# Kernel tuning notes

Hardware: AMD Instinct MI355X
Metric: run time of the kernel (lower is better)

## Reference

```python
import jax, jax.numpy as jnp
import numpy as np


def _conv1x1(x, w, b):
    # x: [B,C,H,W], w: [O,C], b: [O] -> [B,O,H,W]
    return jnp.einsum('bchw,oc->bohw', x, w) + b[None, :, None, None]


def setup_inputs() -> dict:
    key = jax.random.key(0)
    ks = jax.random.split(key, 5)
    B, C, H, W = 4, 256, 64, 64
    C2 = C // 2
    scale = 0.02  # keep attention logits in a sane range
    return {
        'x': jax.random.normal(ks[0], (B, C, H, W), dtype=jnp.float32),
        'w_theta': jax.random.normal(ks[1], (C2, C), dtype=jnp.float32) * scale,
        'b_theta': jnp.zeros((C2,), dtype=jnp.float32),
        'w_phi': jax.random.normal(ks[2], (C2, C), dtype=jnp.float32) * scale,
        'b_phi': jnp.zeros((C2,), dtype=jnp.float32),
        'w_g': jax.random.normal(ks[3], (C2, C), dtype=jnp.float32) * scale,
        'b_g': jnp.zeros((C2,), dtype=jnp.float32),
        'w_out': jax.random.normal(ks[4], (C, C2), dtype=jnp.float32) * scale,
        'b_out': jnp.zeros((C,), dtype=jnp.float32),
    }


def reference(x, w_theta, b_theta, w_phi, b_phi, w_g, b_g, w_out, b_out):
    B, C, H, W = x.shape
    C2 = C // 2
    N = H * W
    theta = _conv1x1(x, w_theta, b_theta).reshape(B, C2, N)  # [B,C2,N]
    phi = _conv1x1(x, w_phi, b_phi).reshape(B, C2, N)        # [B,C2,N]
    g = _conv1x1(x, w_g, b_g).reshape(B, C2, N)              # [B,C2,N]
    # non-local attention: scores[b,m,n] = theta[b,:,m] . phi[b,:,n]
    scores = jnp.einsum('bcm,bcn->bmn', theta, phi)          # [B,N,N]
    attn = jax.nn.softmax(scores, axis=-1)                   # [B,N,N]
    # output = g @ attn^T : out[b,c,m] = sum_n g[b,c,n] * attn[b,m,n]
    out = jnp.einsum('bcn,bmn->bcm', g, attn)                # [B,C2,N]
    out = out.reshape(B, C2, H, W)
    return x + _conv1x1(out, w_out, b_out)
```

## Files before the change

kernel.cpp:

```cpp
#include <hip/hip_runtime.h>
#include <hip/hip_bf16.h>

#define B_  4
#define C_  256
#define C2_ 128
#define N_  4096
#define LOG2E 1.4426950408889634f

typedef unsigned short u16;
typedef __attribute__((ext_vector_type(8))) short bf16x8;
typedef __attribute__((ext_vector_type(4))) float f32x4;

static __device__ __forceinline__ u16 f2bf(float f) {
    return __builtin_bit_cast(u16, __float2bfloat16(f));
}
static __device__ __forceinline__ float bf2f(u16 u) {
    return __bfloat162float(__builtin_bit_cast(__hip_bfloat16, u));
}
static __device__ __forceinline__ bf16x8 cvt8(const float* p) {
    u16 t[8];
#pragma unroll
    for (int j = 0; j < 8; ++j) t[j] = f2bf(p[j]);
    return *(const bf16x8*)t;
}

__global__ __launch_bounds__(256, 2) void projx_kernel(
    const float* __restrict__ x,
    const float* __restrict__ wt, const float* __restrict__ wp,
    const float* __restrict__ wg,
    const float* __restrict__ b_theta, const float* __restrict__ b_phi,
    const float* __restrict__ b_g,
    u16* __restrict__ Q, u16* __restrict__ K, u16* __restrict__ V) {
    __shared__ __align__(16) u16 XTs[64][264];
    __shared__ __align__(16) u16 Ws[64][264];
    u16 (*Vt)[72] = (u16(*)[72])XTs;

    int bid = blockIdx.x;
    int b   = bid / (N_ / 64);
    int n0  = (bid % (N_ / 64)) * 64;
    int tid = threadIdx.x;
    int wave = tid >> 6, lane = tid & 63, quad = (lane >> 4) & 3, l16 = lane & 15;

#pragma unroll
    for (int it = 0; it < 8; ++it) {
        int idx = it * 256 + tid;
        int q = idx & 15, p = idx >> 4;
        const float* r0 = x + ((size_t)b * C_ + 2 * p) * N_ + n0 + 4 * q;
        float4 v0 = *(const float4*)r0;
        float4 v1 = *(const float4*)(r0 + N_);
        const float* f0 = (const float*)&v0;
        const float* f1 = (const float*)&v1;
#pragma unroll
        for (int j = 0; j < 4; ++j) {
            unsigned pk = (unsigned)f2bf(f0[j]) | ((unsigned)f2bf(f1[j]) << 16);
            *(unsigned*)&XTs[4 * q + j][2 * p] = pk;
        }
    }
    __syncthreads();

    bf16x8 af[8];
#pragma unroll
    for (int ks = 0; ks < 8; ++ks)
        af[ks] = *(const bf16x8*)&XTs[wave * 16 + l16][ks * 32 + quad * 8];
    __syncthreads();

    const float* wms[3]    = { wt, wp, wg };
    const float* biases[3] = { b_theta, b_phi, b_g };

#pragma unroll
    for (int mat = 0; mat < 3; ++mat) {
        const float* wm = wms[mat];
        const float* bias = biases[mat];
#pragma unroll
        for (int h = 0; h < 2; ++h) {
#pragma unroll
            for (int it = 0; it < 8; ++it) {
                int idx = it * 256 + tid;
                int row = idx >> 5, c8 = (idx & 31) * 8;
                const float* src = wm + (size_t)(h * 64 + row) * C_ + c8;
                float w8[8];
                *(float4*)&w8[0] = *(const float4*)src;
                *(float4*)&w8[4] = *(const float4*)(src + 4);
                bf16x8 v = cvt8(w8);
                *(bf16x8*)&Ws[row][c8] = v;
            }
            __syncthreads();

            f32x4 acc[4];
#pragma unroll
            for (int i = 0; i < 4; ++i) acc[i] = (f32x4){0.f, 0.f, 0.f, 0.f};
#pragma unroll
            for (int ct = 0; ct < 4; ++ct)
#pragma unroll
                for (int ks = 0; ks < 8; ++ks) {
                    bf16x8 bf = *(const bf16x8*)&Ws[ct * 16 + l16][ks * 32 + quad * 8];
                    acc[ct] = __builtin_amdgcn_mfma_f32_16x16x32_bf16(
                        af[ks], bf, acc[ct], 0, 0, 0);
                }

            if (mat < 2) {
                u16* dst = mat == 0 ? Q : K;
                float sc = mat == 0 ? LOG2E : 1.0f;
#pragma unroll
                for (int ct = 0; ct < 4; ++ct) {
                    int c2 = h * 64 + ct * 16 + l16;
                    float bb = bias[c2];
#pragma unroll
                    for (int r = 0; r < 4; ++r) {
                        int n = n0 + wave * 16 + quad * 4 + r;
                        dst[((size_t)b * N_ + n) * C2_ + c2] =
                            f2bf((acc[ct][r] + bb) * sc);
                    }
                }
            } else {
#pragma unroll
                for (int ct = 0; ct < 4; ++ct) {
                    int c2 = h * 64 + ct * 16 + l16;
                    float bb = bias[c2];
#pragma unroll
                    for (int r = 0; r < 4; ++r)
                        Vt[c2][wave * 16 + quad * 4 + r] = f2bf(acc[ct][r] + bb);
                }
            }
            __syncthreads();
        }
    }

#pragma unroll
    for (int it = 0; it < 4; ++it) {
        int idx = it * 256 + tid;
        int row = idx >> 3, n8 = (idx & 7) * 8;
        *(uint4*)(V + ((size_t)b * C2_ + row) * N_ + n0 + n8) =
            *(const uint4*)&Vt[row][n8];
    }
}

__global__ __launch_bounds__(256, 2) void attn_kernel(
    const u16* __restrict__ Q, const u16* __restrict__ K,
    const u16* __restrict__ V, u16* __restrict__ AO,
    u16* __restrict__ Opb, float* __restrict__ lsum, int nsplit) {
    const int BM = 128, BN = 64, D = C2_;
    const int per = B_ * (N_ / BM);
    int s    = blockIdx.x / per;
    int r0   = blockIdx.x % per;
    int b    = r0 / (N_ / BM);
    int m0   = (r0 % (N_ / BM)) * BM;
    int tid  = threadIdx.x;
    int wave = tid >> 6, lane = tid & 63, quad = (lane >> 4) & 3, l16 = lane & 15;

    __shared__ __align__(16) u16 Ks[BN][D + 8];
    __shared__ __align__(16) u16 Vs[D][BN + 8];
    __shared__ __align__(16) u16 Psb[4][32][BN + 8];
    u16* Ps = &Psb[wave][0][0];

    bf16x8 qf[2][4];
#pragma unroll
    for (int ms = 0; ms < 2; ++ms) {
        const u16* qp = Q + ((size_t)b * N_ + m0 + wave * 32 + ms * 16 + l16) * D;
#pragma unroll
        for (int kk = 0; kk < 4; ++kk)
            qf[ms][kk] = *(const bf16x8*)(qp + kk * 32 + quad * 8);
    }

    float l_r[2][4] = {{0.f, 0.f, 0.f, 0.f}, {0.f, 0.f, 0.f, 0.f}};
    f32x4 o_acc[2][8];
#pragma unroll
    for (int ms = 0; ms < 2; ++ms)
#pragma unroll
        for (int i = 0; i < 8; ++i) o_acc[ms][i] = (f32x4){0.f, 0.f, 0.f, 0.f};

    const int tiles = N_ / BN;
    const int base = tiles / nsplit, rem = tiles % nsplit;
    const int t0 = s * base + (s < rem ? s : rem);
    const int cnt = base + (s < rem ? 1 : 0);
    const int nt0 = t0 * BN, nt1 = (t0 + cnt) * BN;

    for (int nt = nt0; nt < nt1; nt += BN) {
        const u16* kp = K + ((size_t)b * N_ + nt) * D;
#pragma unroll
        for (int it = 0; it < 4; ++it) {
            int idx = it * 256 + tid;
            int row = idx >> 4, col = (idx & 15) * 8;
            *(uint4*)&Ks[row][col] = *(const uint4*)(kp + row * D + col);
        }
#pragma unroll
        for (int it = 0; it < 4; ++it) {
            int idx = it * 256 + tid;
            int row = idx >> 3, col = (idx & 7) * 8;
            *(uint4*)&Vs[row][col] =
                *(const uint4*)(V + ((size_t)b * C2_ + row) * N_ + nt + col);
        }
        __syncthreads();

        f32x4 sc[2][4];
#pragma unroll
        for (int nn = 0; nn < 4; ++nn) {
            f32x4 a0 = (f32x4){0.f, 0.f, 0.f, 0.f};
            f32x4 a1 = (f32x4){0.f, 0.f, 0.f, 0.f};
#pragma unroll
            for (int kk = 0; kk < 4; ++kk) {
                bf16x8 kf = *(const bf16x8*)&Ks[nn * 16 + l16][kk * 32 + quad * 8];
                a0 = __builtin_amdgcn_mfma_f32_16x16x32_bf16(qf[0][kk], kf, a0, 0, 0, 0);
                a1 = __builtin_amdgcn_mfma_f32_16x16x32_bf16(qf[1][kk], kf, a1, 0, 0, 0);
            }
            sc[0][nn] = a0;
            sc[1][nn] = a1;
        }

#pragma unroll
        for (int ms = 0; ms < 2; ++ms)
#pragma unroll
            for (int nn = 0; nn < 4; ++nn)
#pragma unroll
                for (int r = 0; r < 4; ++r) {
                    float p = __builtin_amdgcn_exp2f(sc[ms][nn][r]);
                    l_r[ms][r] += p;
                    Ps[(ms * 16 + quad * 4 + r) * (BN + 8) + nn * 16 + l16] = f2bf(p);
                }

#pragma unroll
        for (int ks = 0; ks < 2; ++ks) {
            bf16x8 pf0 = *(const bf16x8*)&Ps[(l16) * (BN + 8) + ks * 32 + quad * 8];
            bf16x8 pf1 = *(const bf16x8*)&Ps[(16 + l16) * (BN + 8) + ks * 32 + quad * 8];
#pragma unroll
            for (int cs = 0; cs < 8; ++cs) {
                bf16x8 vf = *(const bf16x8*)&Vs[cs * 16 + l16][ks * 32 + quad * 8];
                o_acc[0][cs] = __builtin_amdgcn_mfma_f32_16x16x32_bf16(pf0, vf, o_acc[0][cs], 0, 0, 0);
                o_acc[1][cs] = __builtin_amdgcn_mfma_f32_16x16x32_bf16(pf1, vf, o_acc[1][cs], 0, 0, 0);
            }
        }
        __syncthreads();
    }

#pragma unroll
    for (int ms = 0; ms < 2; ++ms)
#pragma unroll
        for (int r = 0; r < 4; ++r) {
            l_r[ms][r] += __shfl_xor(l_r[ms][r], 1);
            l_r[ms][r] += __shfl_xor(l_r[ms][r], 2);
            l_r[ms][r] += __shfl_xor(l_r[ms][r], 4);
            l_r[ms][r] += __shfl_xor(l_r[ms][r], 8);
        }

    if (Opb) {
#pragma unroll
        for (int ms = 0; ms < 2; ++ms) {
#pragma unroll
            for (int cs = 0; cs < 8; ++cs)
#pragma unroll
                for (int r = 0; r < 4; ++r) {
                    size_t row = (size_t)s * (B_ * N_) + (size_t)b * N_ +
                                 m0 + wave * 32 + ms * 16 + quad * 4 + r;
                    Opb[row * C2_ + cs * 16 + l16] = f2bf(o_acc[ms][cs][r]);
                }
            if (l16 == 0)
#pragma unroll
                for (int r = 0; r < 4; ++r) {
                    size_t row = (size_t)s * (B_ * N_) + (size_t)b * N_ +
                                 m0 + wave * 32 + ms * 16 + quad * 4 + r;
                    lsum[row] = l_r[ms][r];
                }
        }
    } else {
#pragma unroll
        for (int ms = 0; ms < 2; ++ms)
#pragma unroll
            for (int cs = 0; cs < 8; ++cs)
#pragma unroll
                for (int r = 0; r < 4; ++r) {
                    float v = o_acc[ms][cs][r] / l_r[ms][r];
                    AO[((size_t)b * N_ + m0 + wave * 32 + ms * 16 + quad * 4 + r) * C2_ +
                       cs * 16 + l16] = f2bf(v);
                }
    }
}

__global__ __launch_bounds__(256) void outproj_kernel(
    const float* __restrict__ x, const u16* __restrict__ Opb,
    const float* __restrict__ lsum, const u16* __restrict__ AO,
    const float* __restrict__ w_out, const float* __restrict__ b_out,
    float* __restrict__ y, int nsplit) {
    __shared__ __align__(16) u16 As[64][C2_ + 8];
    __shared__ __align__(16) u16 Ws2[64][C2_ + 8];
    __shared__ float Ls[64];
    int bid = blockIdx.x;
    int per_b = (C_ / 64) * (N_ / 64);
    int b   = bid / per_b;
    int rem = bid % per_b;
    int c0  = (rem / (N_ / 64)) * 64;
    int n0  = (rem % (N_ / 64)) * 64;
    int tid = threadIdx.x;
    int wave = tid >> 6, lane = tid & 63, quad = (lane >> 4) & 3, l16 = lane & 15;

#pragma unroll
    for (int it = 0; it < 4; ++it) {
        int idx = it * 256 + tid;
        int row = idx >> 4, c8 = (idx & 15) * 8;
        const float* src = w_out + (size_t)(c0 + row) * C2_ + c8;
        float w8[8];
        *(float4*)&w8[0] = *(const float4*)src;
        *(float4*)&w8[4] = *(const float4*)(src + 4);
        bf16x8 v = cvt8(w8);
        *(bf16x8*)&Ws2[row][c8] = v;
    }

    if (nsplit > 1) {
        if (tid < 64) {
            float L = 0.f;
            for (int s = 0; s < nsplit; ++s)
                L += lsum[(size_t)s * (B_ * N_) + (size_t)b * N_ + n0 + tid];
            Ls[tid] = 1.f / L;
        }
        __syncthreads();
#pragma unroll
        for (int it = 0; it < 4; ++it) {
            int idx = it * 256 + tid;
            int n = idx >> 4, c8 = (idx & 15) * 8;
            float a[8] = {0.f, 0.f, 0.f, 0.f, 0.f, 0.f, 0.f, 0.f};
            for (int s = 0; s < nsplit; ++s) {
                const u16* op = Opb +
                    ((size_t)s * (B_ * N_) + (size_t)b * N_ + n0 + n) * C2_ + c8;
                uint4 raw = *(const uint4*)op;
                const u16* rp = (const u16*)&raw;
#pragma unroll
                for (int j = 0; j < 8; ++j) a[j] += bf2f(rp[j]);
            }
            float inv = Ls[n];
            u16 o[8];
#pragma unroll
            for (int j = 0; j < 8; ++j) o[j] = f2bf(a[j] * inv);
            *(uint4*)&As[n][c8] = *(const uint4*)o;
        }
    } else {
#pragma unroll
        for (int it = 0; it < 4; ++it) {
            int idx = it * 256 + tid;
            int n = idx >> 4, c8 = (idx & 15) * 8;
            *(uint4*)&As[n][c8] =
                *(const uint4*)(AO + ((size_t)b * N_ + n0 + n) * C2_ + c8);
        }
    }
    __syncthreads();

    bf16x8 af[4];
#pragma unroll
    for (int kk = 0; kk < 4; ++kk)
        af[kk] = *(const bf16x8*)&Ws2[wave * 16 + l16][kk * 32 + quad * 8];

    f32x4 acc[4];
#pragma unroll
    for (int i = 0; i < 4; ++i) acc[i] = (f32x4){0.f, 0.f, 0.f, 0.f};

#pragma unroll
    for (int nn = 0; nn < 4; ++nn)
#pragma unroll
        for (int kk = 0; kk < 4; ++kk) {
            bf16x8 bf = *(const bf16x8*)&As[nn * 16 + l16][kk * 32 + quad * 8];
            acc[nn] = __builtin_amdgcn_mfma_f32_16x16x32_bf16(af[kk], bf, acc[nn], 0, 0, 0);
        }

    int cw = c0 + wave * 16;
    float bo[4];
#pragma unroll
    for (int r = 0; r < 4; ++r) bo[r] = b_out[cw + quad * 4 + r];

#pragma unroll
    for (int nn = 0; nn < 4; ++nn)
#pragma unroll
        for (int r = 0; r < 4; ++r) {
            int c = cw + quad * 4 + r;
            size_t off = ((size_t)b * C_ + c) * N_ + n0 + nn * 16 + l16;
            y[off] = x[off] + bo[r] + acc[nn][r];
        }
}

extern "C" void kernel_launch(void* const* d_in, const int* in_sizes, int n_in,
                              void* d_out, int out_size, void* d_ws, size_t ws_size,
                              hipStream_t stream) {
    const float* x       = (const float*)d_in[0];
    const float* w_theta = (const float*)d_in[1];
    const float* b_theta = (const float*)d_in[2];
    const float* w_phi   = (const float*)d_in[3];
    const float* b_phi   = (const float*)d_in[4];
    const float* w_g     = (const float*)d_in[5];
    const float* b_g     = (const float*)d_in[6];
    const float* w_out   = (const float*)d_in[7];
    const float* b_out   = (const float*)d_in[8];
    float* y = (float*)d_out;

    const size_t SZ = (size_t)B_ * N_ * C2_;
    u16* Q = (u16*)d_ws;
    u16* K = Q + SZ;
    u16* V = K + SZ;
    char* dyn = (char*)(V + SZ);
    size_t fixedB = 3 * SZ * 2;

    size_t perS = SZ * 2 + (size_t)B_ * N_ * 4;

    int S;
    if      (ws_size >= fixedB + 4 * perS) S = 4;
    else if (ws_size >= fixedB + 2 * perS) S = 2;
    else                                   S = 1;

    u16*   AO  = (u16*)dyn;
    u16*   Opb = nullptr;
    float* ls  = nullptr;
    if (S > 1) {
        Opb = (u16*)dyn;
        ls  = (float*)(Opb + (size_t)S * SZ);
    }

    projx_kernel<<<B_ * (N_ / 64), 256, 0, stream>>>(
        x, w_theta, w_phi, w_g, b_theta, b_phi, b_g, Q, K, V);
    attn_kernel<<<B_ * (N_ / 128) * S, 256, 0, stream>>>(Q, K, V, AO, Opb, ls, S);
    outproj_kernel<<<B_ * (C_ / 64) * (N_ / 64), 256, 0, stream>>>(
        x, Opb, ls, AO, w_out, b_out, y, S);
}
```

Measured before the change: 154.7 us.

## Split projection over channel halves, swizzle block order, coalesce output stores

```diff
diff --git a/kernel.cpp b/kernel.cpp
--- a/kernel.cpp
+++ b/kernel.cpp
@@ -23,6 +23,8 @@
     for (int j = 0; j < 8; ++j) t[j] = f2bf(p[j]);
     return *(const bf16x8*)t;
 }
+
+#define XW 264
 
 __global__ __launch_bounds__(256, 2) void projx_kernel(
     const float* __restrict__ x,
@@ -31,29 +33,31 @@
     const float* __restrict__ b_theta, const float* __restrict__ b_phi,
     const float* __restrict__ b_g,
     u16* __restrict__ Q, u16* __restrict__ K, u16* __restrict__ V) {
-    __shared__ __align__(16) u16 XTs[64][264];
-    __shared__ __align__(16) u16 Ws[64][264];
+    __shared__ __align__(16) u16 XTs[64][XW];
+    __shared__ __align__(16) u16 Ws[64][XW];
     u16 (*Vt)[72] = (u16(*)[72])XTs;
 
-    int bid = blockIdx.x;
-    int b   = bid / (N_ / 64);
-    int n0  = (bid % (N_ / 64)) * 64;
+    int p = blockIdx.x;
+    int b = (p & 7) >> 1;
+    int j = ((p >> 3) << 1) | (p & 1);
+    int h  = j >> 6;
+    int n0 = (j & 63) * 64;
     int tid = threadIdx.x;
     int wave = tid >> 6, lane = tid & 63, quad = (lane >> 4) & 3, l16 = lane & 15;
 
 #pragma unroll
     for (int it = 0; it < 8; ++it) {
         int idx = it * 256 + tid;
-        int q = idx & 15, p = idx >> 4;
-        const float* r0 = x + ((size_t)b * C_ + 2 * p) * N_ + n0 + 4 * q;
+        int q = idx & 15, pp = idx >> 4;
+        const float* r0 = x + ((size_t)b * C_ + 2 * pp) * N_ + n0 + 4 * q;
         float4 v0 = *(const float4*)r0;
         float4 v1 = *(const float4*)(r0 + N_);
         const float* f0 = (const float*)&v0;
         const float* f1 = (const float*)&v1;
 #pragma unroll
-        for (int j = 0; j < 4; ++j) {
-            unsigned pk = (unsigned)f2bf(f0[j]) | ((unsigned)f2bf(f1[j]) << 16);
-            *(unsigned*)&XTs[4 * q + j][2 * p] = pk;
+        for (int jj = 0; jj < 4; ++jj) {
+            unsigned pk = (unsigned)f2bf(f0[jj]) | ((unsigned)f2bf(f1[jj]) << 16);
+            *(unsigned*)&XTs[4 * q + jj][2 * pp] = pk;
         }
     }
     __syncthreads();
@@ -72,65 +76,61 @@
         const float* wm = wms[mat];
         const float* bias = biases[mat];
 #pragma unroll
-        for (int h = 0; h < 2; ++h) {
-#pragma unroll
-            for (int it = 0; it < 8; ++it) {
-                int idx = it * 256 + tid;
-                int row = idx >> 5, c8 = (idx & 31) * 8;
-                const float* src = wm + (size_t)(h * 64 + row) * C_ + c8;
-                float w8[8];
-                *(float4*)&w8[0] = *(const float4*)src;
-                *(float4*)&w8[4] = *(const float4*)(src + 4);
-                bf16x8 v = cvt8(w8);
-                *(bf16x8*)&Ws[row][c8] = v;
-            }
-            __syncthreads();
-
-            f32x4 acc[4];
-#pragma unroll
-            for (int i = 0; i < 4; ++i) acc[i] = (f32x4){0.f, 0.f, 0.f, 0.f};
-#pragma unroll
-            for (int ct = 0; ct < 4; ++ct)
-#pragma unroll
-                for (int ks = 0; ks < 8; ++ks) {
-                    bf16x8 bf = *(const bf16x8*)&Ws[ct * 16 + l16][ks * 32 + quad * 8];
-                    acc[ct] = __builtin_amdgcn_mfma_f32_16x16x32_bf16(
-                        af[ks], bf, acc[ct], 0, 0, 0);
+        for (int it = 0; it < 8; ++it) {
+            int idx = it * 256 + tid;
+            int row = idx >> 5, c8 = (idx & 31) * 8;
+            const float* src = wm + (size_t)(h * 64 + row) * C_ + c8;
+            float w8[8];
+            *(float4*)&w8[0] = *(const float4*)src;
+            *(float4*)&w8[4] = *(const float4*)(src + 4);
+            *(bf16x8*)&Ws[row][c8] = cvt8(w8);
+        }
+        __syncthreads();
+
+        f32x4 acc[4];
+#pragma unroll
+        for (int i = 0; i < 4; ++i) acc[i] = (f32x4){0.f, 0.f, 0.f, 0.f};
+#pragma unroll
+        for (int ct = 0; ct < 4; ++ct)
+#pragma unroll
+            for (int ks = 0; ks < 8; ++ks) {
+                bf16x8 bf = *(const bf16x8*)&Ws[ct * 16 + l16][ks * 32 + quad * 8];
+                acc[ct] = __builtin_amdgcn_mfma_f32_16x16x32_bf16(
+                    af[ks], bf, acc[ct], 0, 0, 0);
+            }
+
+        if (mat < 2) {
+            u16* dst = mat == 0 ? Q : K;
+            float scl = mat == 0 ? LOG2E : 1.0f;
+#pragma unroll
+            for (int ct = 0; ct < 4; ++ct) {
+                int c2 = h * 64 + ct * 16 + l16;
+                float bb = bias[c2];
+#pragma unroll
+                for (int r = 0; r < 4; ++r) {
+                    int n = n0 + wave * 16 + quad * 4 + r;
+                    dst[((size_t)b * N_ + n) * C2_ + c2] =
+                        f2bf((acc[ct][r] + bb) * scl);
                 }
-
-            if (mat < 2) {
-                u16* dst = mat == 0 ? Q : K;
-                float sc = mat == 0 ? LOG2E : 1.0f;
-#pragma unroll
-                for (int ct = 0; ct < 4; ++ct) {
-                    int c2 = h * 64 + ct * 16 + l16;
-                    float bb = bias[c2];
-#pragma unroll
-                    for (int r = 0; r < 4; ++r) {
-                        int n = n0 + wave * 16 + quad * 4 + r;
-                        dst[((size_t)b * N_ + n) * C2_ + c2] =
-                            f2bf((acc[ct][r] + bb) * sc);
-                    }
-                }
-            } else {
-#pragma unroll
-                for (int ct = 0; ct < 4; ++ct) {
-                    int c2 = h * 64 + ct * 16 + l16;
-                    float bb = bias[c2];
-#pragma unroll
-                    for (int r = 0; r < 4; ++r)
-                        Vt[c2][wave * 16 + quad * 4 + r] = f2bf(acc[ct][r] + bb);
-                }
-            }
-            __syncthreads();
-        }
-    }
-
-#pragma unroll
-    for (int it = 0; it < 4; ++it) {
+            }
+        } else {
+#pragma unroll
+            for (int ct = 0; ct < 4; ++ct) {
+                int c2l = ct * 16 + l16;
+                float bb = bias[h * 64 + c2l];
+#pragma unroll
+                for (int r = 0; r < 4; ++r)
+                    Vt[c2l][wave * 16 + quad * 4 + r] = f2bf(acc[ct][r] + bb);
+            }
+        }
+        __syncthreads();
+    }
+
+#pragma unroll
+    for (int it = 0; it < 2; ++it) {
         int idx = it * 256 + tid;
         int row = idx >> 3, n8 = (idx & 7) * 8;
-        *(uint4*)(V + ((size_t)b * C2_ + row) * N_ + n0 + n8) =
+        *(uint4*)(V + ((size_t)b * C2_ + h * 64 + row) * N_ + n0 + n8) =
             *(const uint4*)&Vt[row][n8];
     }
 }
@@ -140,11 +140,11 @@
     const u16* __restrict__ V, u16* __restrict__ AO,
     u16* __restrict__ Opb, float* __restrict__ lsum, int nsplit) {
     const int BM = 128, BN = 64, D = C2_;
-    const int per = B_ * (N_ / BM);
-    int s    = blockIdx.x / per;
-    int r0   = blockIdx.x % per;
-    int b    = r0 / (N_ / BM);
-    int m0   = (r0 % (N_ / BM)) * BM;
+    int p = blockIdx.x;
+    int b = (p & 7) >> 1;
+    int j = ((p >> 3) << 1) | (p & 1);
+    int s  = j >> 5;
+    int m0 = (j & 31) * BM;
     int tid  = threadIdx.x;
     int wave = tid >> 6, lane = tid & 63, quad = (lane >> 4) & 3, l16 = lane & 15;
 
@@ -213,9 +213,9 @@
             for (int nn = 0; nn < 4; ++nn)
 #pragma unroll
                 for (int r = 0; r < 4; ++r) {
-                    float p = __builtin_amdgcn_exp2f(sc[ms][nn][r]);
-                    l_r[ms][r] += p;
-                    Ps[(ms * 16 + quad * 4 + r) * (BN + 8) + nn * 16 + l16] = f2bf(p);
+                    float pv = __builtin_amdgcn_exp2f(sc[ms][nn][r]);
+                    l_r[ms][r] += pv;
+                    Ps[(ms * 16 + quad * 4 + r) * (BN + 8) + nn * 16 + l16] = f2bf(pv);
                 }
 
 #pragma unroll
@@ -275,20 +275,23 @@
     }
 }
 
-__global__ __launch_bounds__(256) void outproj_kernel(
+#define OW 136
+
+__global__ __launch_bounds__(256, 4) void outproj_kernel(
     const float* __restrict__ x, const u16* __restrict__ Opb,
     const float* __restrict__ lsum, const u16* __restrict__ AO,
     const float* __restrict__ w_out, const float* __restrict__ b_out,
     float* __restrict__ y, int nsplit) {
-    __shared__ __align__(16) u16 As[64][C2_ + 8];
-    __shared__ __align__(16) u16 Ws2[64][C2_ + 8];
+    __shared__ __align__(16) u16 As[64][OW];
+    __shared__ __align__(16) u16 Ws2[64][OW];
     __shared__ float Ls[64];
-    int bid = blockIdx.x;
-    int per_b = (C_ / 64) * (N_ / 64);
-    int b   = bid / per_b;
-    int rem = bid % per_b;
-    int c0  = (rem / (N_ / 64)) * 64;
-    int n0  = (rem % (N_ / 64)) * 64;
+    float (*Yt)[68] = (float(*)[68])&As[0][0];
+
+    int p = blockIdx.x;
+    int b = (p & 7) >> 1;
+    int j = ((p >> 3) << 1) | (p & 1);
+    int c0 = (j >> 6) * 64;
+    int n0 = (j & 63) * 64;
     int tid = threadIdx.x;
     int wave = tid >> 6, lane = tid & 63, quad = (lane >> 4) & 3, l16 = lane & 15;
 
@@ -300,8 +303,7 @@
         float w8[8];
         *(float4*)&w8[0] = *(const float4*)src;
         *(float4*)&w8[4] = *(const float4*)(src + 4);
-        bf16x8 v = cvt8(w8);
-        *(bf16x8*)&Ws2[row][c8] = v;
+        *(bf16x8*)&Ws2[row][c8] = cvt8(w8);
     }
 
     if (nsplit > 1) {
@@ -323,12 +325,12 @@
                 uint4 raw = *(const uint4*)op;
                 const u16* rp = (const u16*)&raw;
 #pragma unroll
-                for (int j = 0; j < 8; ++j) a[j] += bf2f(rp[j]);
+                for (int jj = 0; jj < 8; ++jj) a[jj] += bf2f(rp[jj]);
             }
             float inv = Ls[n];
             u16 o[8];
 #pragma unroll
-            for (int j = 0; j < 8; ++j) o[j] = f2bf(a[j] * inv);
+            for (int jj = 0; jj < 8; ++jj) o[jj] = f2bf(a[jj] * inv);
             *(uint4*)&As[n][c8] = *(const uint4*)o;
         }
     } else {
@@ -364,14 +366,27 @@
 #pragma unroll
     for (int r = 0; r < 4; ++r) bo[r] = b_out[cw + quad * 4 + r];
 
+    __syncthreads();
 #pragma unroll
     for (int nn = 0; nn < 4; ++nn)
 #pragma unroll
-        for (int r = 0; r < 4; ++r) {
-            int c = cw + quad * 4 + r;
-            size_t off = ((size_t)b * C_ + c) * N_ + n0 + nn * 16 + l16;
-            y[off] = x[off] + bo[r] + acc[nn][r];
-        }
+        for (int r = 0; r < 4; ++r)
+            Yt[wave * 16 + quad * 4 + r][nn * 16 + l16] = acc[nn][r] + bo[r];
+    __syncthreads();
+
+    {
+        int row = tid >> 2, sg = (tid & 3) * 16;
+        const float4* xr = (const float4*)(x + ((size_t)b * C_ + c0 + row) * N_ + n0 + sg);
+        float4*       yr = (float4*)(y + ((size_t)b * C_ + c0 + row) * N_ + n0 + sg);
+        const float4* tr = (const float4*)&Yt[row][sg];
+#pragma unroll
+        for (int jj = 0; jj < 4; ++jj) {
+            float4 xv = xr[jj];
+            float4 tv = tr[jj];
+            yr[jj] = make_float4(xv.x + tv.x, xv.y + tv.y,
+                                 xv.z + tv.z, xv.w + tv.w);
+        }
+    }
 }
 
 extern "C" void kernel_launch(void* const* d_in, const int* in_sizes, int n_in,
@@ -410,7 +425,7 @@
         ls  = (float*)(Opb + (size_t)S * SZ);
     }
 
-    projx_kernel<<<B_ * (N_ / 64), 256, 0, stream>>>(
+    projx_kernel<<<B_ * (N_ / 64) * 2, 256, 0, stream>>>(
         x, w_theta, w_phi, w_g, b_theta, b_phi, b_g, Q, K, V);
     attn_kernel<<<B_ * (N_ / 128) * S, 256, 0, stream>>>(Q, K, V, AO, Opb, ls, S);
     outproj_kernel<<<B_ * (C_ / 64) * (N_ / 64), 256, 0, stream>>>(
```

Result: no change. 156.3 us (+1.0%).
